# Kernel optimization log

Hardware: AMD Instinct MI355X
Metric: run time of the kernel (lower is better)

The kernel has to match this reference:

```python
import jax, jax.numpy as jnp
import numpy as np
import math

B, S, D, H = 4, 2048, 1024, 16
DEPTH = D // H


def setup_inputs() -> dict:
    key = jax.random.key(0)
    ks = jax.random.split(key, 8)
    scale = 1.0 / math.sqrt(D)
    return {
        "v": jax.random.normal(ks[0], (B, S, D), dtype=jnp.float32),
        "k": jax.random.normal(ks[1], (B, S, D), dtype=jnp.float32),
        "q": jax.random.normal(ks[2], (B, S, D), dtype=jnp.float32),
        "wq_w": jax.random.normal(ks[3], (D, D), dtype=jnp.float32) * scale,
        "wq_b": jnp.zeros((D,), dtype=jnp.float32),
        "wk_w": jax.random.normal(ks[4], (D, D), dtype=jnp.float32) * scale,
        "wk_b": jnp.zeros((D,), dtype=jnp.float32),
        "wv_w": jax.random.normal(ks[5], (D, D), dtype=jnp.float32) * scale,
        "wv_b": jnp.zeros((D,), dtype=jnp.float32),
        "dense_w": jax.random.normal(ks[6], (D, D), dtype=jnp.float32) * scale,
        "dense_b": jnp.zeros((D,), dtype=jnp.float32),
    }


def _split_heads(x):
    # [B, S, D] -> [B, H, S, depth]
    b, s, _ = x.shape
    return x.reshape(b, s, H, DEPTH).transpose(0, 2, 1, 3)


def reference(v, k, q, wq_w, wq_b, wk_w, wk_b, wv_w, wv_b, dense_w, dense_b):
    # Linear projections (torch Linear: x @ W.T + b)
    qh = _split_heads(q @ wq_w.T + wq_b)
    kh = _split_heads(k @ wk_w.T + wk_b)
    vh = _split_heads(v @ wv_w.T + wv_b)

    # scaled dot-product attention; scores: [B, H, S, S]
    scores = jnp.einsum("bhqd,bhkd->bhqk", qh, kh) / math.sqrt(DEPTH)
    attn = jax.nn.softmax(scores, axis=-1)
    ctx = jnp.einsum("bhqk,bhkd->bhqd", attn, vh)

    # merge heads: [B, H, S, depth] -> [B, S, D]
    ctx = ctx.transpose(0, 2, 1, 3).reshape(q.shape[0], -1, D)
    return ctx @ dense_w.T + dense_b
```

## Files before the change

kernel.cpp:

```cpp
#include <hip/hip_runtime.h>
#include <hip/hip_bf16.h>
#include <stdint.h>

#define B_  4
#define S_  2048
#define D_  1024
#define H_  16
#define DP_ 64
#define M_  (B_*S_)

typedef __bf16 bf16x8 __attribute__((ext_vector_type(8)));
typedef __bf16 bf16x2_t __attribute__((ext_vector_type(2)));
typedef float  f32x4  __attribute__((ext_vector_type(4)));
typedef float  f32x16 __attribute__((ext_vector_type(16)));
typedef float  f32x2_t __attribute__((ext_vector_type(2)));
typedef unsigned short u16x8 __attribute__((ext_vector_type(8)));

struct SwapT  { static constexpr bool v = true;  };
struct NoSwapT{ static constexpr bool v = false; };

__device__ __forceinline__ unsigned short f2bf(float f) {
    __bf16 b = (__bf16)f;
    return __builtin_bit_cast(unsigned short, b);
}
__device__ __forceinline__ unsigned pk_bf16(float lo, float hi) {
    f32x2_t f = {lo, hi};
    bf16x2_t b = __builtin_convertvector(f, bf16x2_t);
    return __builtin_bit_cast(unsigned, b);
}
__device__ __forceinline__ bf16x8 ld_frag(const unsigned short* p) {
    return __builtin_bit_cast(bf16x8, *(const u16x8*)p);
}
__device__ __forceinline__ f32x4 mfma16(bf16x8 a, bf16x8 b, f32x4 c) {
    return __builtin_amdgcn_mfma_f32_16x16x32_bf16(a, b, c, 0, 0, 0);
}
__device__ __forceinline__ f32x16 mfma32(bf16x8 a, bf16x8 b, f32x16 c) {
    return __builtin_amdgcn_mfma_f32_32x32x16_bf16(a, b, c, 0, 0, 0);
}
__device__ __forceinline__ void pl32swap(unsigned &a, unsigned &b) {
    asm volatile("v_permlane32_swap_b32 %0, %1" : "+v"(a), "+v"(b));
}
__device__ __forceinline__ void gl2lds16(const void* g, void* l) {
    __builtin_amdgcn_global_load_lds(
        (const __attribute__((address_space(1))) unsigned*)g,
        (__attribute__((address_space(3))) unsigned*)l, 16, 0, 0);
}

__global__ __launch_bounds__(256)
void cvt_all(const float* __restrict__ w0, const float* __restrict__ w1,
             const float* __restrict__ w2, const float* __restrict__ w3,
             const float* __restrict__ a0, const float* __restrict__ a1,
             const float* __restrict__ a2,
             unsigned short* __restrict__ Wcat, unsigned short* __restrict__ Acat)
{
    const int gid = blockIdx.x * 256 + threadIdx.x;
    const float* src; unsigned short* dst;
    if (gid < 524288) {
        const int wi = gid >> 17;
        const size_t off = (size_t)(gid & 131071) * 8;
        const float* ws[4] = {w0, w1, w2, w3};
        src = ws[wi] + off; dst = Wcat + (size_t)wi * 1048576 + off;
    } else {
        const int g2 = gid - 524288;
        const int ai = g2 >> 20;
        const size_t off = (size_t)(g2 & 1048575) * 8;
        const float* as[3] = {a0, a1, a2};
        src = as[ai] + off; dst = Acat + (size_t)ai * 8388608 + off;
    }
    float4 x = ((const float4*)src)[0];
    float4 y = ((const float4*)src)[1];
    uint4 o;
    o.x = pk_bf16(x.x, x.y); o.y = pk_bf16(x.z, x.w);
    o.z = pk_bf16(y.x, y.y); o.w = pk_bf16(y.z, y.w);
    *(uint4*)dst = o;
}

template<int MODE>
__global__ __launch_bounds__(256)
void gemm_bt(const unsigned short* __restrict__ Acat, size_t a_stride,
             const unsigned short* __restrict__ Wcat,
             const float* __restrict__ bias0, const float* __restrict__ bias1,
             const float* __restrict__ bias2,
             void* __restrict__ Out, void* __restrict__ Out2)
{
    __shared__ __align__(16) unsigned short SM[16384];
    unsigned short* As = SM;
    unsigned short* Bs = SM + 8192;

    const int z = (MODE == 1) ? blockIdx.z : 0;
    const unsigned short* A = Acat + (size_t)z * a_stride;
    const unsigned short* W = Wcat + ((size_t)z << 20);
    const float* bias = (z == 0) ? bias0 : (z == 1 ? bias1 : bias2);

    const int tid  = threadIdx.x;
    const int wave = tid >> 6, lane = tid & 63;
    const int quad = lane >> 4, l16 = lane & 15;
    const int wm = (wave >> 1) * 64, wn = (wave & 1) * 64;
    const int row0 = blockIdx.x * 128, col0 = blockIdx.y * 128;

    const int srow = lane >> 3;
    const int sg   = (lane & 7) ^ srow;

    f32x4 acc[4][4];
#pragma unroll
    for (int i = 0; i < 4; i++)
#pragma unroll
        for (int j = 0; j < 4; j++) acc[i][j] = (f32x4){0.f, 0.f, 0.f, 0.f};

    auto stage = [&](int kt) {
        const int k0 = kt * 64;
#pragma unroll
        for (int j = 0; j < 4; ++j) {
            const int c = wave * 4 + j;
            gl2lds16(A + (size_t)(row0 + c * 8 + srow) * D_ + k0 + sg * 8,
                     (unsigned char*)As + c * 1024);
            gl2lds16(W + (size_t)(col0 + c * 8 + srow) * D_ + k0 + sg * 8,
                     (unsigned char*)Bs + c * 1024);
        }
    };

    auto kloop = [&](auto tag) {
        constexpr bool SW = decltype(tag)::v;
        stage(0);
        for (int kt = 0; kt < D_ / 64; ++kt) {
            __syncthreads();
            bf16x8 af[4][2], bv[4][2];
#pragma unroll
            for (int mi = 0; mi < 4; ++mi) {
                const int row = wm + mi * 16 + l16;
#pragma unroll
                for (int kd = 0; kd < 2; ++kd)
                    af[mi][kd] = ld_frag(&As[row * 64 + (((kd * 4 + quad) ^ (row & 7)) * 8)]);
            }
#pragma unroll
            for (int ni = 0; ni < 4; ++ni) {
                const int row = wn + ni * 16 + l16;
#pragma unroll
                for (int kd = 0; kd < 2; ++kd)
                    bv[ni][kd] = ld_frag(&Bs[row * 64 + (((kd * 4 + quad) ^ (row & 7)) * 8)]);
            }
            if (kt + 1 < D_ / 64) {
                __syncthreads();
                stage(kt + 1);
            }
#pragma unroll
            for (int kd = 0; kd < 2; ++kd)
#pragma unroll
                for (int mi = 0; mi < 4; ++mi)
#pragma unroll
                    for (int ni = 0; ni < 4; ++ni) {
                        if constexpr (SW)
                            acc[mi][ni] = mfma16(bv[ni][kd], af[mi][kd], acc[mi][ni]);
                        else
                            acc[mi][ni] = mfma16(af[mi][kd], bv[ni][kd], acc[mi][ni]);
                    }
        }
    };
    if (MODE == 1 && z < 2) kloop(SwapT{});
    else                    kloop(NoSwapT{});

    if constexpr (MODE == 1) {
        if (z < 2) {
            unsigned short* Lt = SM;
            unsigned short* OutQK = (unsigned short*)Out + ((size_t)z << 23);
            const int bidx = row0 >> 11;
            const float scale = (z == 0) ? 0.18033688f : 1.0f;
#pragma unroll
            for (int hc = 0; hc < 2; ++hc) {
                __syncthreads();
                if ((wave & 1) == hc) {
#pragma unroll
                    for (int ni = 0; ni < 4; ++ni) {
                        const int c_loc = wn + ni * 16 + quad * 4;
                        const float4 bb = *(const float4*)&bias[col0 + c_loc];
#pragma unroll
                        for (int mi = 0; mi < 4; ++mi) {
                            const int s_loc = wm + mi * 16 + l16;
                            uint2 w;
                            w.x = pk_bf16((acc[mi][ni][0] + bb.x) * scale,
                                          (acc[mi][ni][1] + bb.y) * scale);
                            w.y = pk_bf16((acc[mi][ni][2] + bb.z) * scale,
                                          (acc[mi][ni][3] + bb.w) * scale);
                            *(uint2*)&Lt[s_loc * 72 + (c_loc & 63)] = w;
                        }
                    }
                }
                __syncthreads();
                const int hg = (col0 >> 6) + hc;
                const size_t qb = (size_t)(bidx * H_ + hg) * S_ + (row0 & (S_ - 1));
#pragma unroll
                for (int p = 0; p < 4; ++p) {
                    const int s = p * 32 + (tid >> 3);
                    const int g = tid & 7;
                    uint4 d = *(const uint4*)&Lt[s * 72 + g * 8];
                    *(uint4*)(OutQK + (qb + s) * DP_ + g * 8) = d;
                }
            }
        } else {
            unsigned short* Lt = SM;
            unsigned short* OutV = (unsigned short*)Out2;
            const int bidx = row0 >> 11;
#pragma unroll
            for (int hc = 0; hc < 2; ++hc) {
                __syncthreads();
                if ((wave & 1) == hc) {
#pragma unroll
                    for (int ni = 0; ni < 4; ++ni) {
                        const float bvv = bias[col0 + hc * 64 + ni * 16 + l16];
#pragma unroll
                        for (int mi = 0; mi < 4; ++mi) {
                            uint2 w;
                            w.x = pk_bf16(acc[mi][ni][0] + bvv, acc[mi][ni][1] + bvv);
                            w.y = pk_bf16(acc[mi][ni][2] + bvv, acc[mi][ni][3] + bvv);
                            *(uint2*)&Lt[(ni * 16 + l16) * 132 + wm + mi * 16 + quad * 4] = w;
                        }
                    }
                }
                __syncthreads();
                const int hg = (col0 >> 6) + hc;
                const size_t vb = ((size_t)(bidx * H_ + hg) * DP_) * S_;
#pragma unroll
                for (int p = 0; p < 4; ++p) {
                    const int dpl = p * 16 + (tid >> 4);
                    uint4 d = *(const uint4*)&Lt[dpl * 132 + (tid & 15) * 8];
                    *(uint4*)(OutV + vb + (size_t)dpl * S_ + (row0 & (S_ - 1)) + (tid & 15) * 8) = d;
                }
            }
        }
        return;
    }
#pragma unroll
    for (int ni = 0; ni < 4; ni++) {
        const int col = col0 + wn + ni * 16 + l16;
        const float bvv = bias0[col];
#pragma unroll
        for (int mi = 0; mi < 4; mi++) {
            const int rowb = row0 + wm + mi * 16 + quad * 4;
#pragma unroll
            for (int r = 0; r < 4; r++)
                ((float*)Out)[(size_t)(rowb + r) * D_ + col] = acc[mi][ni][r] + bvv;
        }
    }
}

__global__ __launch_bounds__(256)
void flash_attn(const unsigned short* __restrict__ Qh,
                const unsigned short* __restrict__ Kh,
                const unsigned short* __restrict__ Vtg,
                unsigned short* __restrict__ Ctx)
{
    __shared__ __align__(16) unsigned short Kt[128 * 64];
    __shared__ __align__(16) unsigned short Vt[2][64 * 128];

    const int tid  = threadIdx.x;
    const int wave = tid >> 6, lane = tid & 63;
    const int l32 = lane & 31, hi = lane >> 5;
    const int bh = blockIdx.x, qt = blockIdx.y;
    const size_t base = (size_t)bh * S_ * DP_;

    bf16x8 qf[4];
#pragma unroll
    for (int dpc = 0; dpc < 4; ++dpc)
        qf[dpc] = ld_frag(&Qh[base + (size_t)(qt * 128 + wave * 32 + l32) * DP_ + dpc * 16 + hi * 8]);

    f32x16 o[2] = {};
    f32x2_t ls = {0.f, 0.f};

    const int kswz  = ((lane & 7) ^ (lane >> 3)) * 8;
    const int vdp_l = lane >> 4;
    const int vslot = lane & 15;

    auto stageK = [&](int t) {
#pragma unroll
        for (int j = 0; j < 4; ++j) {
            const int ck = wave * 4 + j;
            gl2lds16(Kh + base + (size_t)(t * 128 + ck * 8 + (lane >> 3)) * DP_ + kswz,
                     (unsigned char*)Kt + ck * 1024);
        }
    };
    auto stageV = [&](int t, unsigned short* Vb) {
#pragma unroll
        for (int j = 0; j < 4; ++j) {
            const int ck = wave * 4 + j;
            const int dp = ck * 4 + vdp_l;
            gl2lds16(Vtg + base + (size_t)dp * S_ + t * 128 + ((vslot ^ (dp & 15)) * 8),
                     (unsigned char*)Vb + ck * 1024);
        }
    };

    stageK(0);
    __builtin_amdgcn_sched_barrier(0);
    stageV(0, Vt[0]);

    for (int t = 0; t < S_ / 128; ++t) {
        asm volatile("s_waitcnt vmcnt(4)" ::: "memory");
        __builtin_amdgcn_sched_barrier(0);
        __builtin_amdgcn_s_barrier();

        f32x16 st[4] = {};
        __builtin_amdgcn_s_setprio(1);
#pragma unroll
        for (int kt = 0; kt < 4; ++kt) {
#pragma unroll
            for (int dpc = 0; dpc < 4; ++dpc) {
                bf16x8 kf = ld_frag(&Kt[(kt * 32 + l32) * 64 + ((((dpc << 1) + hi) ^ (l32 & 7)) * 8)]);
                st[kt] = mfma32(kf, qf[dpc], st[kt]);
            }
        }
        __builtin_amdgcn_s_setprio(0);

        asm volatile("s_waitcnt vmcnt(0)" ::: "memory");
        __builtin_amdgcn_sched_barrier(0);
        __builtin_amdgcn_s_barrier();

        if (t + 1 < S_ / 128) {
            stageK(t + 1);
            __builtin_amdgcn_sched_barrier(0);
            stageV(t + 1, Vt[(t + 1) & 1]);
        }

        const unsigned short* Vc = Vt[t & 1];
#pragma unroll
        for (int kt = 0; kt < 4; ++kt) {
            float p[16];
#pragma unroll
            for (int r = 0; r < 16; ++r) p[r] = __builtin_amdgcn_exp2f(st[kt][r]);
#pragma unroll
            for (int r = 0; r < 16; r += 2) ls += (f32x2_t){p[r], p[r + 1]};
            unsigned m[8];
#pragma unroll
            for (int j = 0; j < 8; ++j) m[j] = pk_bf16(p[2 * j], p[2 * j + 1]);
            pl32swap(m[0], m[2]); pl32swap(m[1], m[3]);
            pl32swap(m[4], m[6]); pl32swap(m[5], m[7]);
            __builtin_amdgcn_s_setprio(1);
#pragma unroll
            for (int c = 0; c < 2; ++c) {
                const bf16x8 pa = __builtin_bit_cast(bf16x8,
                    (uint4){m[4 * c], m[4 * c + 1], m[4 * c + 2], m[4 * c + 3]});
#pragma unroll
                for (int nt = 0; nt < 2; ++nt) {
                    const int dp = nt * 32 + l32;
                    bf16x8 vb = ld_frag(&Vc[dp * 128 + ((((kt << 2) + (c << 1) + hi) ^ (dp & 15)) * 8)]);
                    o[nt] = mfma32(pa, vb, o[nt]);
                }
            }
            __builtin_amdgcn_s_setprio(0);
        }
    }

    float lsum = ls[0] + ls[1];
    lsum += __shfl_xor(lsum, 32, 64);
    const float inv = __builtin_amdgcn_rcpf(lsum);

    const int b = bh >> 4, h = bh & 15;
#pragma unroll
    for (int r = 0; r < 16; ++r) {
        const int qrow = (r & 3) + 8 * (r >> 2) + 4 * hi;
        const float invr = __shfl(inv, qrow, 64);
        const int s = qt * 128 + wave * 32 + qrow;
#pragma unroll
        for (int nt = 0; nt < 2; ++nt)
            Ctx[((size_t)(b * S_ + s)) * D_ + h * DP_ + nt * 32 + l32] = f2bf(o[nt][r] * invr);
    }
}

extern "C" void kernel_launch(void* const* d_in, const int* in_sizes, int n_in,
                              void* d_out, int out_size, void* d_ws, size_t ws_size,
                              hipStream_t stream)
{
    const float* v    = (const float*)d_in[0];
    const float* k    = (const float*)d_in[1];
    const float* q    = (const float*)d_in[2];
    const float* wq_w = (const float*)d_in[3];
    const float* wq_b = (const float*)d_in[4];
    const float* wk_w = (const float*)d_in[5];
    const float* wk_b = (const float*)d_in[6];
    const float* wv_w = (const float*)d_in[7];
    const float* wv_b = (const float*)d_in[8];
    const float* dw   = (const float*)d_in[9];
    const float* db   = (const float*)d_in[10];
    float* out = (float*)d_out;

    unsigned short* Qh   = (unsigned short*)d_ws;
    unsigned short* Kh   = Qh   + (size_t)M_ * D_;
    unsigned short* Vt   = Kh   + (size_t)M_ * D_;
    unsigned short* Ctx  = Vt   + (size_t)M_ * D_;
    unsigned short* Wcat = Ctx  + (size_t)M_ * D_;
    unsigned short* Acat = Wcat + (size_t)4 * D_ * D_;

    cvt_all<<<14336, 256, 0, stream>>>(wq_w, wk_w, wv_w, dw, q, k, v, Wcat, Acat);

    dim3 blk(256);
    gemm_bt<1><<<dim3(M_ / 128, D_ / 128, 3), blk, 0, stream>>>(
        Acat, (size_t)M_ * D_, Wcat, wq_b, wk_b, wv_b, Qh, Vt);

    flash_attn<<<dim3(B_ * H_, S_ / 128), blk, 0, stream>>>(Qh, Kh, Vt, Ctx);

    gemm_bt<0><<<dim3(M_ / 128, D_ / 128, 1), blk, 0, stream>>>(
        Ctx, 0, Wcat + (size_t)3 * D_ * D_, db, db, db, out, nullptr);
}
```

Measured before the change: 333.1 us.

## Single-buffer V tile and fuse exp/pack into QK^T loop in flash attention

Shrinks the V shared-memory tile from double to single buffering and moves the exp2/bf16 packing of scores into the QK^T loop, so each score tile is turned into packed P fragments right after its MFMAs. The K prefetch is issued before the PV MFMAs, while the V prefetch now waits for an extra barrier after PV finishes. This lowers LDS use and score register pressure, which may allow higher occupancy. The cost is less overlap of the V load with compute and one more barrier per iteration.

```diff
diff --git a/kernel.cpp b/kernel.cpp
--- a/kernel.cpp
+++ b/kernel.cpp
@@ -250,7 +250,7 @@
                 unsigned short* __restrict__ Ctx)
 {
     __shared__ __align__(16) unsigned short Kt[128 * 64];
-    __shared__ __align__(16) unsigned short Vt[2][64 * 128];
+    __shared__ __align__(16) unsigned short Vt[64 * 128];
 
     const int tid  = threadIdx.x;
     const int wave = tid >> 6, lane = tid & 63;
@@ -278,74 +278,70 @@
                      (unsigned char*)Kt + ck * 1024);
         }
     };
-    auto stageV = [&](int t, unsigned short* Vb) {
+    auto stageV = [&](int t) {
 #pragma unroll
         for (int j = 0; j < 4; ++j) {
             const int ck = wave * 4 + j;
             const int dp = ck * 4 + vdp_l;
             gl2lds16(Vtg + base + (size_t)dp * S_ + t * 128 + ((vslot ^ (dp & 15)) * 8),
-                     (unsigned char*)Vb + ck * 1024);
+                     (unsigned char*)Vt + ck * 1024);
         }
     };
 
     stageK(0);
     __builtin_amdgcn_sched_barrier(0);
-    stageV(0, Vt[0]);
+    stageV(0);
 
     for (int t = 0; t < S_ / 128; ++t) {
         asm volatile("s_waitcnt vmcnt(4)" ::: "memory");
         __builtin_amdgcn_sched_barrier(0);
         __builtin_amdgcn_s_barrier();
 
-        f32x16 st[4] = {};
+        unsigned m[4][8];
         __builtin_amdgcn_s_setprio(1);
 #pragma unroll
         for (int kt = 0; kt < 4; ++kt) {
+            f32x16 st = {};
 #pragma unroll
             for (int dpc = 0; dpc < 4; ++dpc) {
                 bf16x8 kf = ld_frag(&Kt[(kt * 32 + l32) * 64 + ((((dpc << 1) + hi) ^ (l32 & 7)) * 8)]);
-                st[kt] = mfma32(kf, qf[dpc], st[kt]);
-            }
+                st = mfma32(kf, qf[dpc], st);
+            }
+#pragma unroll
+            for (int j = 0; j < 8; ++j) {
+                float e0 = __builtin_amdgcn_exp2f(st[2 * j]);
+                float e1 = __builtin_amdgcn_exp2f(st[2 * j + 1]);
+                ls += (f32x2_t){e0, e1};
+                m[kt][j] = pk_bf16(e0, e1);
+            }
+            pl32swap(m[kt][0], m[kt][2]); pl32swap(m[kt][1], m[kt][3]);
+            pl32swap(m[kt][4], m[kt][6]); pl32swap(m[kt][5], m[kt][7]);
         }
         __builtin_amdgcn_s_setprio(0);
 
         asm volatile("s_waitcnt vmcnt(0)" ::: "memory");
         __builtin_amdgcn_sched_barrier(0);
         __builtin_amdgcn_s_barrier();
-
-        if (t + 1 < S_ / 128) {
-            stageK(t + 1);
-            __builtin_amdgcn_sched_barrier(0);
-            stageV(t + 1, Vt[(t + 1) & 1]);
-        }
-
-        const unsigned short* Vc = Vt[t & 1];
-#pragma unroll
-        for (int kt = 0; kt < 4; ++kt) {
-            float p[16];
-#pragma unroll
-            for (int r = 0; r < 16; ++r) p[r] = __builtin_amdgcn_exp2f(st[kt][r]);
-#pragma unroll
-            for (int r = 0; r < 16; r += 2) ls += (f32x2_t){p[r], p[r + 1]};
-            unsigned m[8];
-#pragma unroll
-            for (int j = 0; j < 8; ++j) m[j] = pk_bf16(p[2 * j], p[2 * j + 1]);
-            pl32swap(m[0], m[2]); pl32swap(m[1], m[3]);
-            pl32swap(m[4], m[6]); pl32swap(m[5], m[7]);
-            __builtin_amdgcn_s_setprio(1);
+        if (t + 1 < S_ / 128) stageK(t + 1);
+
+        __builtin_amdgcn_s_setprio(1);
+#pragma unroll
+        for (int kt = 0; kt < 4; ++kt)
 #pragma unroll
             for (int c = 0; c < 2; ++c) {
                 const bf16x8 pa = __builtin_bit_cast(bf16x8,
-                    (uint4){m[4 * c], m[4 * c + 1], m[4 * c + 2], m[4 * c + 3]});
+                    (uint4){m[kt][4 * c], m[kt][4 * c + 1], m[kt][4 * c + 2], m[kt][4 * c + 3]});
 #pragma unroll
                 for (int nt = 0; nt < 2; ++nt) {
                     const int dp = nt * 32 + l32;
-                    bf16x8 vb = ld_frag(&Vc[dp * 128 + ((((kt << 2) + (c << 1) + hi) ^ (dp & 15)) * 8)]);
+                    bf16x8 vb = ld_frag(&Vt[dp * 128 + ((((kt << 2) + (c << 1) + hi) ^ (dp & 15)) * 8)]);
                     o[nt] = mfma32(pa, vb, o[nt]);
                 }
             }
-            __builtin_amdgcn_s_setprio(0);
-        }
+        __builtin_amdgcn_s_setprio(0);
+
+        __builtin_amdgcn_s_barrier();
+        if (t + 1 < S_ / 128) stageV(t + 1);
     }
 
     float lsum = ls[0] + ls[1];
```

Result: no change. 337.0 us (+1.2%).
